# Performance work log

Measured on AMD Instinct MI355X. Metric: run time of the kernel, lower is better.

Reference implementation:

```python
import jax, jax.numpy as jnp
import numpy as np

D, H, W = 160, 192, 160


def _grid_sample_3d(vol, grid):
    """torch F.grid_sample (3D, bilinear/trilinear, padding='zeros', align_corners=False).
    vol: [B,C,D,H,W]; grid: [B,Do,Ho,Wo,3], last dim ordered (x,y,z) in [-1,1]."""
    B, C, Dv, Hv, Wv = vol.shape
    x, y, z = grid[..., 0], grid[..., 1], grid[..., 2]
    # align_corners=False unnormalization
    ix = ((x + 1.0) * Wv - 1.0) * 0.5
    iy = ((y + 1.0) * Hv - 1.0) * 0.5
    iz = ((z + 1.0) * Dv - 1.0) * 0.5
    fx, fy, fz = jnp.floor(ix), jnp.floor(iy), jnp.floor(iz)
    wx, wy, wz = ix - fx, iy - fy, iz - fz
    ix0, iy0, iz0 = fx.astype(jnp.int32), fy.astype(jnp.int32), fz.astype(jnp.int32)
    vol_flat = vol.reshape(B, C, Dv * Hv * Wv)
    out_sp = x.shape[1:]  # (Do, Ho, Wo)

    def gather(zi, yi, xi):
        inb = ((zi >= 0) & (zi < Dv) & (yi >= 0) & (yi < Hv) & (xi >= 0) & (xi < Wv))
        lin = ((jnp.clip(zi, 0, Dv - 1) * Hv + jnp.clip(yi, 0, Hv - 1)) * Wv
               + jnp.clip(xi, 0, Wv - 1)).reshape(B, -1)
        vals = jax.vmap(lambda v, i: v[:, i])(vol_flat, lin)  # [B,C,N]
        return vals.reshape((B, C) + out_sp) * inb[:, None].astype(vol.dtype)

    out = jnp.zeros((B, C) + tuple(out_sp), vol.dtype)
    # fixed 8-corner trilinear accumulation
    for dz, wz_ in ((0, 1.0 - wz), (1, wz)):
        for dy, wy_ in ((0, 1.0 - wy), (1, wy)):
            for dx, wx_ in ((0, 1.0 - wx), (1, wx)):
                w = (wz_ * wy_ * wx_)[:, None]  # [B,1,Do,Ho,Wo]
                out = out + w * gather(iz0 + dz, iy0 + dy, ix0 + dx)
    return out


def _voxel_grid():
    gd, gh, gw = jnp.meshgrid(jnp.arange(D, dtype=jnp.float32),
                              jnp.arange(H, dtype=jnp.float32),
                              jnp.arange(W, dtype=jnp.float32), indexing='ij')
    return jnp.stack([gd, gh, gw])[None]  # [1,3,D,H,W], channels (d,h,w)


def _to_xyz(t):
    # [B,3,D,H,W] channels (d,h,w) -> [B,D,H,W,3] channels (x,y,z)
    return jnp.moveaxis(t, 1, -1)[..., ::-1]


def setup_inputs() -> dict:
    key = jax.random.key(0)
    k1, k2, k3 = jax.random.split(key, 3)
    src = jax.random.normal(k1, (1, 1, D, H, W), dtype=jnp.float32)
    flow1 = jax.random.normal(k2, (1, 3, D, H, W), dtype=jnp.float32)
    flow2 = jax.random.normal(k3, (1, 3, D, H, W), dtype=jnp.float32)
    range_flow = jnp.float32(0.4)
    return {"src": src, "flow1": flow1, "flow2": flow2, "range_flow": range_flow}


def reference(src, flow1, flow2, range_flow):
    grid = _voxel_grid()  # voxel-coordinate identity grid
    # NOTE: grid2 is intentionally NOT normalized to [-1,1] (faithful to source quirk)
    grid2 = _to_xyz(grid + flow2 * range_flow)
    flow1_warped = _grid_sample_3d(flow1, grid2)
    out_flow = flow1_warped + flow2
    denom = jnp.array([D - 1, H - 1, W - 1], jnp.float32).reshape(1, 3, 1, 1, 1)
    new_locs_total = 2.0 * ((grid + out_flow * range_flow) / denom - 0.5)
    deform_2_img = _grid_sample_3d(src, _to_xyz(new_locs_total))
    return deform_2_img, out_flow
```

## Files before the change

kernel.cpp:

```cpp
#include <hip/hip_runtime.h>

constexpr int Dv = 160, Hv = 192, Wv = 160;
constexpr int NN = Dv * Hv * Wv;
constexpr int N4 = NN / 4;

__device__ __forceinline__ float tri1(const float* __restrict__ v,
                                      float ix, float iy, float iz) {
  float fx = floorf(ix), fy = floorf(iy), fz = floorf(iz);
  float wx = ix - fx, wy = iy - fy, wz = iz - fz;
  int x0 = (int)fx, y0 = (int)fy, z0 = (int)fz;
  int x1 = x0 + 1, y1 = y0 + 1, z1 = z0 + 1;
  float wx0 = ((unsigned)x0 < (unsigned)Wv) ? (1.0f - wx) : 0.0f;
  float wx1 = ((unsigned)x1 < (unsigned)Wv) ? wx : 0.0f;
  float wy0 = ((unsigned)y0 < (unsigned)Hv) ? (1.0f - wy) : 0.0f;
  float wy1 = ((unsigned)y1 < (unsigned)Hv) ? wy : 0.0f;
  float wz0 = ((unsigned)z0 < (unsigned)Dv) ? (1.0f - wz) : 0.0f;
  float wz1 = ((unsigned)z1 < (unsigned)Dv) ? wz : 0.0f;
  int xa0 = min(max(x0, 0), Wv - 1), xa1 = min(max(x1, 0), Wv - 1);
  int ya0 = min(max(y0, 0), Hv - 1), ya1 = min(max(y1, 0), Hv - 1);
  int za0 = min(max(z0, 0), Dv - 1), za1 = min(max(z1, 0), Dv - 1);
  int r00 = (za0 * Hv + ya0) * Wv;
  int r01 = (za0 * Hv + ya1) * Wv;
  int r10 = (za1 * Hv + ya0) * Wv;
  int r11 = (za1 * Hv + ya1) * Wv;
  float v000 = v[r00 + xa0], v001 = v[r00 + xa1];
  float v010 = v[r01 + xa0], v011 = v[r01 + xa1];
  float v100 = v[r10 + xa0], v101 = v[r10 + xa1];
  float v110 = v[r11 + xa0], v111 = v[r11 + xa1];
  float c00 = v000 * wx0 + v001 * wx1;
  float c01 = v010 * wx0 + v011 * wx1;
  float c10 = v100 * wx0 + v101 * wx1;
  float c11 = v110 * wx0 + v111 * wx1;
  float c0 = c00 * wy0 + c01 * wy1;
  float c1 = c10 * wy0 + c11 * wy1;
  return c0 * wz0 + c1 * wz1;
}

__device__ __forceinline__ void tri3_rare(const float* __restrict__ v,
                                          float gx, float gy, float gz,
                                          float& o0, float& o1, float& o2) {
  o0 = 0.0f; o1 = 0.0f; o2 = 0.0f;
  float ix = ((gx + 1.0f) * (float)Wv - 1.0f) * 0.5f;
  float iy = ((gy + 1.0f) * (float)Hv - 1.0f) * 0.5f;
  float iz = ((gz + 1.0f) * (float)Dv - 1.0f) * 0.5f;
  float fx = floorf(ix), fy = floorf(iy), fz = floorf(iz);
  int x0 = (int)fx, y0 = (int)fy, z0 = (int)fz;
  if (x0 < -1 || x0 >= Wv || y0 < -1 || y0 >= Hv || z0 < -1 || z0 >= Dv)
    return;
  float wx = ix - fx, wy = iy - fy, wz = iz - fz;
#pragma unroll
  for (int c = 0; c < 8; ++c) {
    const int dz = (c >> 2) & 1, dy = (c >> 1) & 1, dx = c & 1;
    int zi = z0 + dz, yi = y0 + dy, xi = x0 + dx;
    if ((unsigned)zi < (unsigned)Dv && (unsigned)yi < (unsigned)Hv &&
        (unsigned)xi < (unsigned)Wv) {
      float wgt = (dz ? wz : 1.0f - wz) * (dy ? wy : 1.0f - wy) *
                  (dx ? wx : 1.0f - wx);
      int lin = (zi * Hv + yi) * Wv + xi;
      o0 += wgt * v[lin];
      o1 += wgt * v[NN + lin];
      o2 += wgt * v[2 * NN + lin];
    }
  }
}

__global__ __launch_bounds__(256)
void st_fused4_kernel(const float* __restrict__ src,
                      const float* __restrict__ flow1,
                      const float* __restrict__ flow2,
                      const float* __restrict__ rfp,
                      float* __restrict__ out) {
  int t4 = blockIdx.x * blockDim.x + threadIdx.x;
  if (t4 >= N4) return;
  const float rf = rfp[0];

  int idx = t4 << 2;
  int w0 = idx % Wv;
  int tt = idx / Wv;
  int h = tt % Hv;
  int d = tt / Hv;

  float4 f2d = *(const float4*)(flow2 + idx);
  float4 f2h = *(const float4*)(flow2 + NN + idx);
  float4 f2w = *(const float4*)(flow2 + 2 * NN + idx);

  float f20[4] = {f2d.x, f2d.y, f2d.z, f2d.w};
  float f21[4] = {f2h.x, f2h.y, f2h.z, f2h.w};
  float f22[4] = {f2w.x, f2w.y, f2w.z, f2w.w};

  float of0[4], of1[4], of2[4], img[4];

#pragma unroll
  for (int j = 0; j < 4; ++j) {
    float wj = (float)(w0 + j);
    float gx = wj + rf * f22[j];
    float gy = (float)h + rf * f21[j];
    float gz = (float)d + rf * f20[j];

    float a0, a1, a2;
    tri3_rare(flow1, gx, gy, gz, a0, a1, a2);

    of0[j] = a0 + f20[j];
    of1[j] = a1 + f21[j];
    of2[j] = a2 + f22[j];

    float nld = 2.0f * (((float)d + of0[j] * rf) / (float)(Dv - 1) - 0.5f);
    float nlh = 2.0f * (((float)h + of1[j] * rf) / (float)(Hv - 1) - 0.5f);
    float nlw = 2.0f * ((wj + of2[j] * rf) / (float)(Wv - 1) - 0.5f);

    float ix = ((nlw + 1.0f) * (float)Wv - 1.0f) * 0.5f;
    float iy = ((nlh + 1.0f) * (float)Hv - 1.0f) * 0.5f;
    float iz = ((nld + 1.0f) * (float)Dv - 1.0f) * 0.5f;
    img[j] = tri1(src, ix, iy, iz);
  }

  *(float4*)(out + idx)          = make_float4(img[0], img[1], img[2], img[3]);
  *(float4*)(out + NN + idx)     = make_float4(of0[0], of0[1], of0[2], of0[3]);
  *(float4*)(out + 2 * NN + idx) = make_float4(of1[0], of1[1], of1[2], of1[3]);
  *(float4*)(out + 3 * NN + idx) = make_float4(of2[0], of2[1], of2[2], of2[3]);
}

extern "C" void kernel_launch(void* const* d_in, const int* in_sizes, int n_in,
                              void* d_out, int out_size, void* d_ws, size_t ws_size,
                              hipStream_t stream) {
  const float* src   = (const float*)d_in[0];
  const float* flow1 = (const float*)d_in[1];
  const float* flow2 = (const float*)d_in[2];
  const float* rfp   = (const float*)d_in[3];
  float* out = (float*)d_out;

  const int threads = 256;
  const int blocks = (N4 + threads - 1) / threads;
  hipLaunchKernelGGL(st_fused4_kernel, dim3(blocks), dim3(threads), 0, stream,
                     src, flow1, flow2, rfp, out);
}
```

Measured before the change: 199.4 us.

## Stage src halo tile in LDS via async global_load_lds for trilinear gather

Reorganizes the kernel into 3D blocks of 32x8x8 voxels, each thread handling a column of 8 depths. The block loads a source halo tile (tile plus 3-voxel margin) into shared memory with the direct global-to-LDS load builtin, and serves the second trilinear sample from LDS when the 8 corners fall inside the tile, falling back to global gathers otherwise. Coordinate math is also simplified algebraically. This trades vectorized float4 I/O for scalar coalesced loads and stores and adds a barrier plus halo overfetch per block, aiming to cut scattered global gather traffic for src.

Result: faster. 185.4 us (-7.0%).

```diff
diff --git a/kernel.cpp b/kernel.cpp
--- a/kernel.cpp
+++ b/kernel.cpp
@@ -2,39 +2,12 @@
 
 constexpr int Dv = 160, Hv = 192, Wv = 160;
 constexpr int NN = Dv * Hv * Wv;
-constexpr int N4 = NN / 4;
 
-__device__ __forceinline__ float tri1(const float* __restrict__ v,
-                                      float ix, float iy, float iz) {
-  float fx = floorf(ix), fy = floorf(iy), fz = floorf(iz);
-  float wx = ix - fx, wy = iy - fy, wz = iz - fz;
-  int x0 = (int)fx, y0 = (int)fy, z0 = (int)fz;
-  int x1 = x0 + 1, y1 = y0 + 1, z1 = z0 + 1;
-  float wx0 = ((unsigned)x0 < (unsigned)Wv) ? (1.0f - wx) : 0.0f;
-  float wx1 = ((unsigned)x1 < (unsigned)Wv) ? wx : 0.0f;
-  float wy0 = ((unsigned)y0 < (unsigned)Hv) ? (1.0f - wy) : 0.0f;
-  float wy1 = ((unsigned)y1 < (unsigned)Hv) ? wy : 0.0f;
-  float wz0 = ((unsigned)z0 < (unsigned)Dv) ? (1.0f - wz) : 0.0f;
-  float wz1 = ((unsigned)z1 < (unsigned)Dv) ? wz : 0.0f;
-  int xa0 = min(max(x0, 0), Wv - 1), xa1 = min(max(x1, 0), Wv - 1);
-  int ya0 = min(max(y0, 0), Hv - 1), ya1 = min(max(y1, 0), Hv - 1);
-  int za0 = min(max(z0, 0), Dv - 1), za1 = min(max(z1, 0), Dv - 1);
-  int r00 = (za0 * Hv + ya0) * Wv;
-  int r01 = (za0 * Hv + ya1) * Wv;
-  int r10 = (za1 * Hv + ya0) * Wv;
-  int r11 = (za1 * Hv + ya1) * Wv;
-  float v000 = v[r00 + xa0], v001 = v[r00 + xa1];
-  float v010 = v[r01 + xa0], v011 = v[r01 + xa1];
-  float v100 = v[r10 + xa0], v101 = v[r10 + xa1];
-  float v110 = v[r11 + xa0], v111 = v[r11 + xa1];
-  float c00 = v000 * wx0 + v001 * wx1;
-  float c01 = v010 * wx0 + v011 * wx1;
-  float c10 = v100 * wx0 + v101 * wx1;
-  float c11 = v110 * wx0 + v111 * wx1;
-  float c0 = c00 * wy0 + c01 * wy1;
-  float c1 = c10 * wy0 + c11 * wy1;
-  return c0 * wz0 + c1 * wz1;
-}
+constexpr int TW = 32, TH = 8, TD = 8;
+constexpr int SX = TW + 7, SY = TH + 7, SZ = TD + 7;
+constexpr int SLEN = SX * SY * SZ;
+constexpr int SITER = (SLEN + 255) / 256;
+constexpr int SPAD = SITER * 256;
 
 __device__ __forceinline__ void tri3_rare(const float* __restrict__ v,
                                           float gx, float gy, float gz,
@@ -65,59 +38,128 @@
 }
 
 __global__ __launch_bounds__(256)
-void st_fused4_kernel(const float* __restrict__ src,
-                      const float* __restrict__ flow1,
-                      const float* __restrict__ flow2,
-                      const float* __restrict__ rfp,
-                      float* __restrict__ out) {
-  int t4 = blockIdx.x * blockDim.x + threadIdx.x;
-  if (t4 >= N4) return;
+void st_tiled_kernel(const float* __restrict__ src,
+                     const float* __restrict__ flow1,
+                     const float* __restrict__ flow2,
+                     const float* __restrict__ rfp,
+                     float* __restrict__ out) {
+  __shared__ float tile[SPAD];
+
+  const int tid = threadIdx.x;
+  const int bx0 = blockIdx.x * TW;
+  const int by0 = blockIdx.y * TH;
+  const int bz0 = blockIdx.z * TD;
   const float rf = rfp[0];
 
-  int idx = t4 << 2;
-  int w0 = idx % Wv;
-  int tt = idx / Wv;
-  int h = tt % Hv;
-  int d = tt / Hv;
+  const int lw = tid & (TW - 1);
+  const int lh = tid >> 5;
+  const int w = bx0 + lw;
+  const int h = by0 + lh;
 
-  float4 f2d = *(const float4*)(flow2 + idx);
-  float4 f2h = *(const float4*)(flow2 + NN + idx);
-  float4 f2w = *(const float4*)(flow2 + 2 * NN + idx);
+  float f2d[TD], f2h[TD], f2w[TD];
+#pragma unroll
+  for (int ld = 0; ld < TD; ++ld) {
+    int idx = ((bz0 + ld) * Hv + h) * Wv + w;
+    f2d[ld] = flow2[idx];
+    f2h[ld] = flow2[NN + idx];
+    f2w[ld] = flow2[2 * NN + idx];
+  }
 
-  float f20[4] = {f2d.x, f2d.y, f2d.z, f2d.w};
-  float f21[4] = {f2h.x, f2h.y, f2h.z, f2h.w};
-  float f22[4] = {f2w.x, f2w.y, f2w.z, f2w.w};
+  const int bxo = bx0 - 3, byo = by0 - 3, bzo = bz0 - 3;
+#pragma unroll
+  for (int i = 0; i < SITER; ++i) {
+    int t = tid + i * 256;
+    int tt = min(t, SLEN - 1);
+    int tz = tt / (SY * SX);
+    int r = tt - tz * (SY * SX);
+    int ty = r / SX;
+    int tx = r - ty * SX;
+    int gx = min(max(bxo + tx, 0), Wv - 1);
+    int gy = min(max(byo + ty, 0), Hv - 1);
+    int gz = min(max(bzo + tz, 0), Dv - 1);
+    int g = (gz * Hv + gy) * Wv + gx;
+    __builtin_amdgcn_global_load_lds(
+        (const __attribute__((address_space(1))) void*)(src + g),
+        (__attribute__((address_space(3))) void*)(tile + t), 4, 0, 0);
+  }
+  __syncthreads();
 
-  float of0[4], of1[4], of2[4], img[4];
+  const float wf = (float)w, hf = (float)h;
+  constexpr float KX = (float)Wv / (float)(Wv - 1);
+  constexpr float KY = (float)Hv / (float)(Hv - 1);
+  constexpr float KZ = (float)Dv / (float)(Dv - 1);
 
 #pragma unroll
-  for (int j = 0; j < 4; ++j) {
-    float wj = (float)(w0 + j);
-    float gx = wj + rf * f22[j];
-    float gy = (float)h + rf * f21[j];
-    float gz = (float)d + rf * f20[j];
+  for (int ld = 0; ld < TD; ++ld) {
+    const int d = bz0 + ld;
+    const float df = (float)d;
+    const int idx = (d * Hv + h) * Wv + w;
 
     float a0, a1, a2;
-    tri3_rare(flow1, gx, gy, gz, a0, a1, a2);
+    tri3_rare(flow1, wf + rf * f2w[ld], hf + rf * f2h[ld], df + rf * f2d[ld],
+              a0, a1, a2);
 
-    of0[j] = a0 + f20[j];
-    of1[j] = a1 + f21[j];
-    of2[j] = a2 + f22[j];
+    float of_d = a0 + f2d[ld];
+    float of_h = a1 + f2h[ld];
+    float of_w = a2 + f2w[ld];
 
-    float nld = 2.0f * (((float)d + of0[j] * rf) / (float)(Dv - 1) - 0.5f);
-    float nlh = 2.0f * (((float)h + of1[j] * rf) / (float)(Hv - 1) - 0.5f);
-    float nlw = 2.0f * ((wj + of2[j] * rf) / (float)(Wv - 1) - 0.5f);
+    out[NN + idx] = of_d;
+    out[2 * NN + idx] = of_h;
+    out[3 * NN + idx] = of_w;
 
-    float ix = ((nlw + 1.0f) * (float)Wv - 1.0f) * 0.5f;
-    float iy = ((nlh + 1.0f) * (float)Hv - 1.0f) * 0.5f;
-    float iz = ((nld + 1.0f) * (float)Dv - 1.0f) * 0.5f;
-    img[j] = tri1(src, ix, iy, iz);
+    float ix = (wf + rf * of_w) * KX - 0.5f;
+    float iy = (hf + rf * of_h) * KY - 0.5f;
+    float iz = (df + rf * of_d) * KZ - 0.5f;
+
+    float fx = floorf(ix), fy = floorf(iy), fz = floorf(iz);
+    float wx = ix - fx, wy = iy - fy, wz = iz - fz;
+    int x0 = (int)fx, y0 = (int)fy, z0 = (int)fz;
+
+    float wx0 = ((unsigned)x0 < (unsigned)Wv) ? (1.0f - wx) : 0.0f;
+    float wx1 = ((unsigned)(x0 + 1) < (unsigned)Wv) ? wx : 0.0f;
+    float wy0 = ((unsigned)y0 < (unsigned)Hv) ? (1.0f - wy) : 0.0f;
+    float wy1 = ((unsigned)(y0 + 1) < (unsigned)Hv) ? wy : 0.0f;
+    float wz0 = ((unsigned)z0 < (unsigned)Dv) ? (1.0f - wz) : 0.0f;
+    float wz1 = ((unsigned)(z0 + 1) < (unsigned)Dv) ? wz : 0.0f;
+
+    int tx = x0 - bxo, ty = y0 - byo, tz = z0 - bzo;
+    bool fast = ((unsigned)tx <= (unsigned)(SX - 2)) &
+                ((unsigned)ty <= (unsigned)(SY - 2)) &
+                ((unsigned)tz <= (unsigned)(SZ - 2));
+
+    float v000, v001, v010, v011, v100, v101, v110, v111;
+    if (fast) {
+      int base = (tz * SY + ty) * SX + tx;
+      v000 = tile[base];
+      v001 = tile[base + 1];
+      v010 = tile[base + SX];
+      v011 = tile[base + SX + 1];
+      v100 = tile[base + SY * SX];
+      v101 = tile[base + SY * SX + 1];
+      v110 = tile[base + SY * SX + SX];
+      v111 = tile[base + SY * SX + SX + 1];
+    } else {
+      int xa0 = min(max(x0, 0), Wv - 1), xa1 = min(max(x0 + 1, 0), Wv - 1);
+      int ya0 = min(max(y0, 0), Hv - 1), ya1 = min(max(y0 + 1, 0), Hv - 1);
+      int za0 = min(max(z0, 0), Dv - 1), za1 = min(max(z0 + 1, 0), Dv - 1);
+      int r00 = (za0 * Hv + ya0) * Wv;
+      int r01 = (za0 * Hv + ya1) * Wv;
+      int r10 = (za1 * Hv + ya0) * Wv;
+      int r11 = (za1 * Hv + ya1) * Wv;
+      v000 = src[r00 + xa0]; v001 = src[r00 + xa1];
+      v010 = src[r01 + xa0]; v011 = src[r01 + xa1];
+      v100 = src[r10 + xa0]; v101 = src[r10 + xa1];
+      v110 = src[r11 + xa0]; v111 = src[r11 + xa1];
+    }
+
+    float c00 = v000 * wx0 + v001 * wx1;
+    float c01 = v010 * wx0 + v011 * wx1;
+    float c10 = v100 * wx0 + v101 * wx1;
+    float c11 = v110 * wx0 + v111 * wx1;
+    float c0 = c00 * wy0 + c01 * wy1;
+    float c1 = c10 * wy0 + c11 * wy1;
+    out[idx] = c0 * wz0 + c1 * wz1;
   }
-
-  *(float4*)(out + idx)          = make_float4(img[0], img[1], img[2], img[3]);
-  *(float4*)(out + NN + idx)     = make_float4(of0[0], of0[1], of0[2], of0[3]);
-  *(float4*)(out + 2 * NN + idx) = make_float4(of1[0], of1[1], of1[2], of1[3]);
-  *(float4*)(out + 3 * NN + idx) = make_float4(of2[0], of2[1], of2[2], of2[3]);
 }
 
 extern "C" void kernel_launch(void* const* d_in, const int* in_sizes, int n_in,
@@ -129,8 +171,7 @@
   const float* rfp   = (const float*)d_in[3];
   float* out = (float*)d_out;
 
-  const int threads = 256;
-  const int blocks = (N4 + threads - 1) / threads;
-  hipLaunchKernelGGL(st_fused4_kernel, dim3(blocks), dim3(threads), 0, stream,
+  dim3 grid(Wv / TW, Hv / TH, Dv / TD);
+  hipLaunchKernelGGL(st_tiled_kernel, grid, dim3(256), 0, stream,
                      src, flow1, flow2, rfp, out);
 }
```
